# Kernel optimization log

Hardware: AMD Instinct MI355X
Metric: run time of the kernel (lower is better)

Reference implementation:

```python
import jax, jax.numpy as jnp
import numpy as np

H, W = 200, 200           # BEV spatial shape (single level)
NBQ, NH, NL, NP = 2, 8, 1, 4
D = 256
HD = D // NH


def setup_inputs() -> dict:
    key = jax.random.key(0)
    ks = jax.random.split(key, 12)
    bs, nq = 1, H * W
    query = jax.random.normal(ks[0], (bs, nq, D), jnp.float32)
    value = jax.random.normal(ks[1], (bs, NBQ * nq, D), jnp.float32)
    reference_points = jax.random.uniform(ks[2], (bs, nq, NL, 2), dtype=jnp.float32)
    spatial_shapes = jnp.array([[H, W]], dtype=jnp.int32)
    sc = 1.0 / np.sqrt(D)
    W_v = jax.random.normal(ks[3], (D, D), jnp.float32) * sc
    b_v = jax.random.normal(ks[4], (D,), jnp.float32) * 0.01
    W_so = jax.random.normal(ks[5], (2 * D, NBQ * NH * NL * NP * 2), jnp.float32) * 0.02
    b_so = jax.random.normal(ks[6], (NBQ * NH * NL * NP * 2,), jnp.float32) * 0.5
    W_aw = jax.random.normal(ks[7], (2 * D, NBQ * NH * NL * NP), jnp.float32) * 0.02
    b_aw = jax.random.normal(ks[8], (NBQ * NH * NL * NP,), jnp.float32) * 0.01
    W_o = jax.random.normal(ks[9], (D, D), jnp.float32) * sc
    b_o = jax.random.normal(ks[10], (D,), jnp.float32) * 0.01
    return {"query": query, "value": value, "reference_points": reference_points,
            "spatial_shapes": spatial_shapes,
            "W_v": W_v, "b_v": b_v, "W_so": W_so, "b_so": b_so,
            "W_aw": W_aw, "b_aw": b_aw, "W_o": W_o, "b_o": b_o}


def _ms_deform_attn(value, locs, attn):
    # value: (B, K, NH, HD); locs: (B, nq, NH, NL, NP, 2) in [0,1]; attn: (B, nq, NH, NL, NP)
    B, K, h, d = value.shape
    nq = locs.shape[1]
    out = jnp.zeros((B, nq, h, d), value.dtype)
    start = 0
    for l, (Hl, Wl) in enumerate([(H, W)]):
        v = value[:, start:start + Hl * Wl].transpose(0, 2, 1, 3).reshape(B * h, Hl * Wl, d)
        start += Hl * Wl
        g = locs[:, :, :, l]                      # (B, nq, h, NP, 2)
        # grid_sample(align_corners=False, padding='zeros') pixel coords
        x = g[..., 0] * Wl - 0.5
        y = g[..., 1] * Hl - 0.5
        x0 = jnp.floor(x); y0 = jnp.floor(y)
        lx = x - x0; ly = y - y0
        x0 = x0.astype(jnp.int32); y0 = y0.astype(jnp.int32)
        acc = jnp.zeros((B * h, nq * NP, d), value.dtype)
        for dy, wy in ((0, 1.0 - ly), (1, ly)):
            for dx, wx in ((0, 1.0 - lx), (1, lx)):
                xi = x0 + dx; yi = y0 + dy
                valid = ((xi >= 0) & (xi < Wl) & (yi >= 0) & (yi < Hl)).astype(value.dtype)
                idx = jnp.clip(yi, 0, Hl - 1) * Wl + jnp.clip(xi, 0, Wl - 1)  # (B,nq,h,NP)
                idxf = idx.transpose(0, 2, 1, 3).reshape(B * h, nq * NP)
                samp = jnp.take_along_axis(v, idxf[:, :, None], axis=1)       # (B*h, nq*NP, d)
                wgt = (wx * wy * valid).transpose(0, 2, 1, 3).reshape(B * h, nq * NP, 1)
                acc = acc + samp * wgt
        acc = acc.reshape(B, h, nq, NP, d)
        out = out + jnp.einsum('bhqpd,bqhp->bqhd', acc, attn[:, :, :, l])
    return out.reshape(B, nq, h * d)


def reference(query, value, reference_points, spatial_shapes,
              W_v, b_v, W_so, b_so, W_aw, b_aw, W_o, b_o):
    bs, nq, _ = query.shape
    identity = query
    val4 = value.reshape(bs, NBQ, nq, D)
    # query enhanced with most recent bev-queue features
    qe = jnp.concatenate([val4[:, 0], query], axis=-1)           # (bs, nq, 2D)
    vproj = (value @ W_v + b_v).reshape(bs * NBQ, nq, NH, HD)
    off = (qe @ W_so + b_so).reshape(bs, nq, NH, NBQ, NL, NP, 2)
    aw = (qe @ W_aw + b_aw).reshape(bs, nq, NH, NBQ, NL * NP)
    aw = jax.nn.softmax(aw, axis=-1).reshape(bs, nq, NH, NBQ, NL, NP)
    aw = aw.transpose(0, 3, 1, 2, 4, 5).reshape(bs * NBQ, nq, NH, NL, NP)
    # offset normalizer: [W, H] per level
    norm = jnp.stack([spatial_shapes[:, 1], spatial_shapes[:, 0]], -1).astype(query.dtype)  # (NL,2)
    locs = (reference_points[:, :, None, None, :, None, :]
            + off / norm[None, None, None, None, :, None, :])     # (bs,nq,NH,NBQ,NL,NP,2)
    locs = locs.transpose(0, 3, 1, 2, 4, 5, 6).reshape(bs * NBQ, nq, NH, NL, NP, 2)
    out = _ms_deform_attn(vproj, locs, aw)                        # (bs*NBQ, nq, D)
    out = out.reshape(bs, NBQ, nq, D).mean(axis=1)
    return out @ W_o + b_o + identity
```

## Files before the change

kernel.cpp:

```cpp
#include <hip/hip_runtime.h>
#include <math.h>

#define HW_   40000
#define NQ_   40000
#define IMGW  200
#define IMGH  200

typedef __bf16 bf16;
typedef __attribute__((ext_vector_type(4))) __bf16 bf16x4;
typedef __attribute__((ext_vector_type(8))) __bf16 bf16x8;
typedef __attribute__((ext_vector_type(4))) float f32x4;

__device__ __forceinline__ void gload_lds16(const void* g, void* l) {
  __builtin_amdgcn_global_load_lds(
      (const __attribute__((address_space(1))) void*)g,
      (__attribute__((address_space(3))) void*)l, 16, 0, 0);
}

__global__ __launch_bounds__(256) void cast_f32_bf16_kernel(
    const float* __restrict__ src, bf16* __restrict__ dst, int n8)
{
  int i = blockIdx.x * 256 + threadIdx.x;
  if (i >= n8) return;
  const float4 a = ((const float4*)src)[2 * i];
  const float4 b = ((const float4*)src)[2 * i + 1];
  bf16x8 o = {(bf16)a.x, (bf16)a.y, (bf16)a.z, (bf16)a.w,
              (bf16)b.x, (bf16)b.y, (bf16)b.z, (bf16)b.w};
  *(bf16x8*)&dst[(size_t)i * 8] = o;
}

__global__ __launch_bounds__(256) void cast_transpose_kernel(
    const float* __restrict__ B, bf16* __restrict__ Bt, int K, int N, int ldt)
{
  int idx = blockIdx.x * 256 + threadIdx.x;
  if (idx >= K * N) return;
  int k = idx / N, n = idx - k * N;
  Bt[(size_t)n * ldt + k] = (bf16)B[idx];
}

template<int KT, int MODE>
__global__ __launch_bounds__(256) void mfma_gemm_kernel(
    const bf16* __restrict__ A0, const bf16* __restrict__ A1,
    const bf16* __restrict__ Bt,
    const float* __restrict__ bias0, const float* __restrict__ bias1,
    const float* __restrict__ resid,
    void* __restrict__ outp, void* __restrict__ outp2,
    int M, int N)
{
  __shared__ bf16 As[128 * 32];
  __shared__ bf16 Bs[128 * 32];
  const int t    = threadIdx.x;
  const int m0   = blockIdx.y * 128;
  const int n0   = blockIdx.x * 128;
  const int w    = t >> 6;
  const int lane = t & 63;
  const int quad = lane >> 4;
  const int l16  = lane & 15;
  const int wm   = (w & 1) * 64;
  const int wn   = (w >> 1) * 64;

  f32x4 acc[4][4] = {};

  const int srow  = t >> 2;
  const int skoff = (t & 3) * 8;
  bf16* ldsA0 = As + t * 8;
  bf16* ldsA1 = As + 2048 + t * 8;
  bf16* ldsB0 = Bs + t * 8;
  bf16* ldsB1 = Bs + 2048 + t * 8;

  int gmA0 = m0 + srow;      if (gmA0 >= M) gmA0 = M - 1;
  int gmA1 = m0 + 64 + srow; if (gmA1 >= M) gmA1 = M - 1;
  int gnB0 = n0 + srow;      if (gnB0 >= N) gnB0 = N - 1;
  int gnB1 = n0 + 64 + srow; if (gnB1 >= N) gnB1 = N - 1;

  for (int kt = 0; kt < KT; kt += 32) {
    const bf16* Ap;
    int col;
    if (KT == 512) { Ap = (kt < 256) ? A0 : A1; col = kt & 255; }
    else           { Ap = A0; col = kt; }
    __syncthreads();
    gload_lds16(&Ap[(size_t)gmA0 * 256 + col + skoff], ldsA0);
    gload_lds16(&Ap[(size_t)gmA1 * 256 + col + skoff], ldsA1);
    gload_lds16(&Bt[(size_t)gnB0 * KT + kt + skoff], ldsB0);
    gload_lds16(&Bt[(size_t)gnB1 * KT + kt + skoff], ldsB1);
    __syncthreads();

    bf16x8 af[4], bfr[4];
#pragma unroll
    for (int x = 0; x < 4; ++x) {
      af[x]  = *(const bf16x8*)&As[(wm + x * 16 + l16) * 32 + quad * 8];
      bfr[x] = *(const bf16x8*)&Bs[(wn + x * 16 + l16) * 32 + quad * 8];
    }
#pragma unroll
    for (int mt = 0; mt < 4; ++mt)
#pragma unroll
      for (int nt = 0; nt < 4; ++nt)
        acc[mt][nt] = __builtin_amdgcn_mfma_f32_16x16x32_bf16(
            af[mt], bfr[nt], acc[mt][nt], 0, 0, 0);
  }

#pragma unroll
  for (int mt = 0; mt < 4; ++mt) {
#pragma unroll
    for (int r = 0; r < 4; ++r) {
      const int gm = m0 + wm + mt * 16 + quad * 4 + r;
      if (gm >= M) continue;
#pragma unroll
      for (int nt = 0; nt < 4; ++nt) {
        const int gn = n0 + wn + nt * 16 + l16;
        float v = acc[mt][nt][r];
        if (MODE == 0) {
          int nbq = (gm >= HW_) ? 1 : 0;
          int pix = gm - nbq * HW_;
          int h = gn >> 5, hd = gn & 31;
          ((bf16*)outp)[(((size_t)(nbq * 8 + h) * HW_ + pix) << 5) + hd] =
              (bf16)(v + bias0[gn]);
        } else if (MODE == 1) {
          if (gn < 128)
            ((bf16*)outp)[(size_t)gm * 128 + gn] = (bf16)(v + bias0[gn]);
          else if (gn < 192)
            ((bf16*)outp2)[(size_t)gm * 64 + (gn - 128)] =
                (bf16)(v + bias1[gn - 128]);
        } else {
          ((float*)outp)[(size_t)gm * 256 + gn] =
              v + bias0[gn] + resid[(size_t)gm * 256 + gn];
        }
      }
    }
  }
}

__global__ __launch_bounds__(256) void deform_attn_kernel(
    const bf16* __restrict__ vws,
    const bf16* __restrict__ off_bf,
    const bf16* __restrict__ aw_bf,
    const float* __restrict__ ref,
    bf16* __restrict__ ms)
{
  const int t    = threadIdx.x;
  const int w    = t >> 6;
  const int lane = t & 63;
  const int q    = blockIdx.x * 4 + w;
  const int g    = lane >> 2;
  const int sub  = lane & 3;
  const int h    = g >> 1;
  const int nbq  = g & 1;

  const float rx = ref[2 * q + 0] * (float)IMGW - 0.5f;
  const float ry = ref[2 * q + 1] * (float)IMGH - 0.5f;

  bf16x4 a4 = *(const bf16x4*)&aw_bf[(size_t)q * 64 + g * 4];
  float aa0 = (float)a4[0], aa1 = (float)a4[1], aa2 = (float)a4[2], aa3 = (float)a4[3];
  float mx = fmaxf(fmaxf(aa0, aa1), fmaxf(aa2, aa3));
  float e0 = __expf(aa0 - mx), e1 = __expf(aa1 - mx);
  float e2 = __expf(aa2 - mx), e3 = __expf(aa3 - mx);
  float inv = 1.0f / (e0 + e1 + e2 + e3);
  float w4[4] = {e0 * inv, e1 * inv, e2 * inv, e3 * inv};

  bf16x8 o8 = *(const bf16x8*)&off_bf[(size_t)q * 128 + g * 8];
  float ox[4] = {(float)o8[0], (float)o8[2], (float)o8[4], (float)o8[6]};
  float oy[4] = {(float)o8[1], (float)o8[3], (float)o8[5], (float)o8[7]};

  const bf16* vbase = vws + (((size_t)(nbq * 8 + h) * HW_) << 5) + sub * 8;

  float acc[8] = {};
#pragma unroll
  for (int p = 0; p < 4; ++p) {
    float x = rx + ox[p];
    float y = ry + oy[p];
    float xf = floorf(x), yf = floorf(y);
    int   x0 = (int)xf,   y0 = (int)yf;
    float lx = x - xf,    ly = y - yf;
    int   x1 = x0 + 1,    y1 = y0 + 1;
    float w00 = (1.0f - lx) * (1.0f - ly);
    float w01 = lx * (1.0f - ly);
    float w10 = (1.0f - lx) * ly;
    float w11 = lx * ly;
    if (x0 < 0 || x0 >= IMGW) { w00 = 0.0f; w10 = 0.0f; }
    if (x1 < 0 || x1 >= IMGW) { w01 = 0.0f; w11 = 0.0f; }
    if (y0 < 0 || y0 >= IMGH) { w00 = 0.0f; w01 = 0.0f; }
    if (y1 < 0 || y1 >= IMGH) { w10 = 0.0f; w11 = 0.0f; }
    int xc0 = min(max(x0, 0), IMGW - 1), xc1 = min(max(x1, 0), IMGW - 1);
    int yc0 = min(max(y0, 0), IMGH - 1), yc1 = min(max(y1, 0), IMGH - 1);
    bf16x8 v00 = *(const bf16x8*)&vbase[(size_t)(yc0 * IMGW + xc0) << 5];
    bf16x8 v01 = *(const bf16x8*)&vbase[(size_t)(yc0 * IMGW + xc1) << 5];
    bf16x8 v10 = *(const bf16x8*)&vbase[(size_t)(yc1 * IMGW + xc0) << 5];
    bf16x8 v11 = *(const bf16x8*)&vbase[(size_t)(yc1 * IMGW + xc1) << 5];
    float wp = w4[p];
#pragma unroll
    for (int j = 0; j < 8; ++j) {
      float s = w00 * (float)v00[j] + w01 * (float)v01[j] +
                w10 * (float)v10[j] + w11 * (float)v11[j];
      acc[j] = fmaf(wp, s, acc[j]);
    }
  }

#pragma unroll
  for (int j = 0; j < 8; ++j) acc[j] += __shfl_xor(acc[j], 4);

  if (nbq == 0) {
    bf16x8 o;
#pragma unroll
    for (int j = 0; j < 8; ++j) o[j] = (bf16)(0.5f * acc[j]);
    *(bf16x8*)&ms[(size_t)q * 256 + h * 32 + sub * 8] = o;
  }
}

extern "C" void kernel_launch(void* const* d_in, const int* in_sizes, int n_in,
                              void* d_out, int out_size, void* d_ws, size_t ws_size,
                              hipStream_t stream) {
  const float* query = (const float*)d_in[0];
  const float* value = (const float*)d_in[1];
  const float* ref   = (const float*)d_in[2];
  const float* Wv  = (const float*)d_in[4];
  const float* bv  = (const float*)d_in[5];
  const float* Wso = (const float*)d_in[6];
  const float* bso = (const float*)d_in[7];
  const float* Waw = (const float*)d_in[8];
  const float* baw = (const float*)d_in[9];
  const float* Wo  = (const float*)d_in[10];
  const float* bo  = (const float*)d_in[11];
  float* out = (float*)d_out;

  char* p = (char*)d_ws;
  bf16* vws    = (bf16*)p; p += (size_t)2 * 8 * HW_ * 32 * 2;
  bf16* off_bf = (bf16*)p; p += (size_t)NQ_ * 128 * 2;
  bf16* aw_bf  = (bf16*)p; p += (size_t)NQ_ * 64 * 2;
  bf16* ms     = (bf16*)p; p += (size_t)NQ_ * 256 * 2;
  bf16* vbf    = (bf16*)p; p += (size_t)2 * HW_ * 256 * 2;
  bf16* qbf    = (bf16*)p; p += (size_t)NQ_ * 256 * 2;
  bf16* BtV    = (bf16*)p; p += (size_t)256 * 256 * 2;
  bf16* BtOA   = (bf16*)p; p += (size_t)192 * 512 * 2;
  bf16* BtO    = (bf16*)p; p += (size_t)256 * 256 * 2;

  cast_f32_bf16_kernel<<<10000, 256, 0, stream>>>(value, vbf, 2 * HW_ * 256 / 8);
  cast_f32_bf16_kernel<<<5000, 256, 0, stream>>>(query, qbf, NQ_ * 256 / 8);
  cast_transpose_kernel<<<256, 256, 0, stream>>>(Wv, BtV, 256, 256, 256);
  cast_transpose_kernel<<<256, 256, 0, stream>>>(Wso, BtOA, 512, 128, 512);
  cast_transpose_kernel<<<128, 256, 0, stream>>>(Waw, BtOA + (size_t)128 * 512, 512, 64, 512);
  cast_transpose_kernel<<<256, 256, 0, stream>>>(Wo, BtO, 256, 256, 256);

  mfma_gemm_kernel<256, 0><<<dim3(2, 625), 256, 0, stream>>>(
      vbf, nullptr, BtV, bv, nullptr, nullptr, vws, nullptr, 2 * HW_, 256);
  mfma_gemm_kernel<512, 1><<<dim3(2, 313), 256, 0, stream>>>(
      vbf, qbf, BtOA, bso, baw, nullptr, off_bf, aw_bf, NQ_, 192);
  deform_attn_kernel<<<10000, 256, 0, stream>>>(vws, off_bf, aw_bf, ref, ms);
  mfma_gemm_kernel<256, 2><<<dim3(2, 313), 256, 0, stream>>>(
      ms, nullptr, BtO, bo, nullptr, query, out, nullptr, NQ_, 256);
}
```

Baseline: 340.1 us.

## Merge prep casts into one kernel and double-buffer GEMM LDS loads

Replaces six small cast and cast-transpose launches with one prep kernel that dispatches on block index, removing launch overhead. The MFMA GEMM gains double-buffered LDS tiles, so the next K-slice's global-to-LDS loads are issued before computing on the current one, with a single barrier per iteration. Launch bounds now request 4 blocks per CU. The extra LDS per block and the occupancy hint could limit residency or add register pressure.

```diff
diff --git a/kernel.cpp b/kernel.cpp
--- a/kernel.cpp
+++ b/kernel.cpp
@@ -17,29 +17,46 @@
       (__attribute__((address_space(3))) void*)l, 16, 0, 0);
 }
 
-__global__ __launch_bounds__(256) void cast_f32_bf16_kernel(
-    const float* __restrict__ src, bf16* __restrict__ dst, int n8)
+__global__ __launch_bounds__(256) void prep_kernel(
+    const float* __restrict__ value, const float* __restrict__ query,
+    const float* __restrict__ Wv, const float* __restrict__ Wso,
+    const float* __restrict__ Waw, const float* __restrict__ Wo,
+    bf16* __restrict__ vbf, bf16* __restrict__ qbf,
+    bf16* __restrict__ BtV, bf16* __restrict__ BtOA, bf16* __restrict__ BtO)
 {
-  int i = blockIdx.x * 256 + threadIdx.x;
-  if (i >= n8) return;
-  const float4 a = ((const float4*)src)[2 * i];
-  const float4 b = ((const float4*)src)[2 * i + 1];
-  bf16x8 o = {(bf16)a.x, (bf16)a.y, (bf16)a.z, (bf16)a.w,
-              (bf16)b.x, (bf16)b.y, (bf16)b.z, (bf16)b.w};
-  *(bf16x8*)&dst[(size_t)i * 8] = o;
-}
-
-__global__ __launch_bounds__(256) void cast_transpose_kernel(
-    const float* __restrict__ B, bf16* __restrict__ Bt, int K, int N, int ldt)
-{
-  int idx = blockIdx.x * 256 + threadIdx.x;
-  if (idx >= K * N) return;
-  int k = idx / N, n = idx - k * N;
-  Bt[(size_t)n * ldt + k] = (bf16)B[idx];
+  const int b = blockIdx.x;
+  if (b < 15000) {
+    const float* src = (b < 10000) ? value : query;
+    bf16* dst        = (b < 10000) ? vbf : qbf;
+    int i = (b < 10000 ? b : b - 10000) * 256 + threadIdx.x;
+    const float4 a = ((const float4*)src)[2 * i];
+    const float4 c = ((const float4*)src)[2 * i + 1];
+    bf16x8 o = {(bf16)a.x, (bf16)a.y, (bf16)a.z, (bf16)a.w,
+                (bf16)c.x, (bf16)c.y, (bf16)c.z, (bf16)c.w};
+    *(bf16x8*)&dst[(size_t)i * 8] = o;
+    return;
+  }
+  int idx = (b - 15000) * 256 + threadIdx.x;
+  if (idx < 65536) {
+    int k = idx >> 8, n = idx & 255;
+    BtV[(size_t)n * 256 + k] = (bf16)Wv[idx];
+  } else if (idx < 131072) {
+    int j = idx - 65536;
+    int k = j >> 7, n = j & 127;
+    BtOA[(size_t)n * 512 + k] = (bf16)Wso[j];
+  } else if (idx < 163840) {
+    int j = idx - 131072;
+    int k = j >> 6, n = j & 63;
+    BtOA[(size_t)(128 + n) * 512 + k] = (bf16)Waw[j];
+  } else if (idx < 229376) {
+    int j = idx - 163840;
+    int k = j >> 8, n = j & 255;
+    BtO[(size_t)n * 256 + k] = (bf16)Wo[j];
+  }
 }
 
 template<int KT, int MODE>
-__global__ __launch_bounds__(256) void mfma_gemm_kernel(
+__global__ __launch_bounds__(256, 4) void mfma_gemm_kernel(
     const bf16* __restrict__ A0, const bf16* __restrict__ A1,
     const bf16* __restrict__ Bt,
     const float* __restrict__ bias0, const float* __restrict__ bias1,
@@ -47,8 +64,8 @@
     void* __restrict__ outp, void* __restrict__ outp2,
     int M, int N)
 {
-  __shared__ bf16 As[128 * 32];
-  __shared__ bf16 Bs[128 * 32];
+  __shared__ bf16 As[2][128 * 32];
+  __shared__ bf16 Bs[2][128 * 32];
   const int t    = threadIdx.x;
   const int m0   = blockIdx.y * 128;
   const int n0   = blockIdx.x * 128;
@@ -63,33 +80,36 @@
 
   const int srow  = t >> 2;
   const int skoff = (t & 3) * 8;
-  bf16* ldsA0 = As + t * 8;
-  bf16* ldsA1 = As + 2048 + t * 8;
-  bf16* ldsB0 = Bs + t * 8;
-  bf16* ldsB1 = Bs + 2048 + t * 8;
 
   int gmA0 = m0 + srow;      if (gmA0 >= M) gmA0 = M - 1;
   int gmA1 = m0 + 64 + srow; if (gmA1 >= M) gmA1 = M - 1;
   int gnB0 = n0 + srow;      if (gnB0 >= N) gnB0 = N - 1;
   int gnB1 = n0 + 64 + srow; if (gnB1 >= N) gnB1 = N - 1;
 
-  for (int kt = 0; kt < KT; kt += 32) {
+  auto issue = [&](int kt, int buf) {
     const bf16* Ap;
     int col;
     if (KT == 512) { Ap = (kt < 256) ? A0 : A1; col = kt & 255; }
     else           { Ap = A0; col = kt; }
+    gload_lds16(&Ap[(size_t)gmA0 * 256 + col + skoff], &As[buf][t * 8]);
+    gload_lds16(&Ap[(size_t)gmA1 * 256 + col + skoff], &As[buf][2048 + t * 8]);
+    gload_lds16(&Bt[(size_t)gnB0 * KT + kt + skoff], &Bs[buf][t * 8]);
+    gload_lds16(&Bt[(size_t)gnB1 * KT + kt + skoff], &Bs[buf][2048 + t * 8]);
+  };
+
+  constexpr int NIT = KT / 32;
+  issue(0, 0);
+#pragma unroll
+  for (int it = 0; it < NIT; ++it) {
     __syncthreads();
-    gload_lds16(&Ap[(size_t)gmA0 * 256 + col + skoff], ldsA0);
-    gload_lds16(&Ap[(size_t)gmA1 * 256 + col + skoff], ldsA1);
-    gload_lds16(&Bt[(size_t)gnB0 * KT + kt + skoff], ldsB0);
-    gload_lds16(&Bt[(size_t)gnB1 * KT + kt + skoff], ldsB1);
-    __syncthreads();
-
+    if (it + 1 < NIT) issue((it + 1) * 32, (it + 1) & 1);
+    const bf16* as = As[it & 1];
+    const bf16* bs = Bs[it & 1];
     bf16x8 af[4], bfr[4];
 #pragma unroll
     for (int x = 0; x < 4; ++x) {
-      af[x]  = *(const bf16x8*)&As[(wm + x * 16 + l16) * 32 + quad * 8];
-      bfr[x] = *(const bf16x8*)&Bs[(wn + x * 16 + l16) * 32 + quad * 8];
+      af[x]  = *(const bf16x8*)&as[(wm + x * 16 + l16) * 32 + quad * 8];
+      bfr[x] = *(const bf16x8*)&bs[(wn + x * 16 + l16) * 32 + quad * 8];
     }
 #pragma unroll
     for (int mt = 0; mt < 4; ++mt)
@@ -233,12 +253,8 @@
   bf16* BtOA   = (bf16*)p; p += (size_t)192 * 512 * 2;
   bf16* BtO    = (bf16*)p; p += (size_t)256 * 256 * 2;
 
-  cast_f32_bf16_kernel<<<10000, 256, 0, stream>>>(value, vbf, 2 * HW_ * 256 / 8);
-  cast_f32_bf16_kernel<<<5000, 256, 0, stream>>>(query, qbf, NQ_ * 256 / 8);
-  cast_transpose_kernel<<<256, 256, 0, stream>>>(Wv, BtV, 256, 256, 256);
-  cast_transpose_kernel<<<256, 256, 0, stream>>>(Wso, BtOA, 512, 128, 512);
-  cast_transpose_kernel<<<128, 256, 0, stream>>>(Waw, BtOA + (size_t)128 * 512, 512, 64, 512);
-  cast_transpose_kernel<<<256, 256, 0, stream>>>(Wo, BtO, 256, 256, 256);
+  prep_kernel<<<15896, 256, 0, stream>>>(value, query, Wv, Wso, Waw, Wo,
+                                         vbf, qbf, BtV, BtOA, BtO);
 
   mfma_gemm_kernel<256, 0><<<dim3(2, 625), 256, 0, stream>>>(
       vbf, nullptr, BtV, bv, nullptr, nullptr, vws, nullptr, 2 * HW_, 256);
```

New measurement: 332.0 us. -2.4%, faster.
